# Performance work log

Measured on AMD Instinct MI355X. Metric: run time of the kernel, lower is better.

The kernel has to match this reference:

```python
import jax, jax.numpy as jnp
import numpy as np

B, S, D, H = 4, 2048, 512, 8
HD = D // H  # head dim = 64


def setup_inputs() -> dict:
    key = jax.random.key(0)
    ks = jax.random.split(key, 7)
    s = 0.02
    return {
        "X": jax.random.normal(ks[0], (B, S, D), dtype=jnp.float32),
        "Y": jax.random.normal(ks[1], (B, S, D), dtype=jnp.float32),
        "Z": jax.random.normal(ks[2], (B, S, D), dtype=jnp.float32),
        # weights stored as [in, out] (torch Linear weight transposed)
        "Wq": jax.random.normal(ks[3], (D, D), dtype=jnp.float32) * s,
        "Wk": jax.random.normal(ks[4], (D, D), dtype=jnp.float32) * s,
        "Wv": jax.random.normal(ks[5], (D, D), dtype=jnp.float32) * s,  # dead in original forward
        "Wo": jax.random.normal(ks[6], (D, D), dtype=jnp.float32) * s,
    }


def _split_heads(t):
    # [B, S, D] -> [B, H, S, HD]
    return t.reshape(B, S, H, HD).transpose(0, 2, 1, 3)


def reference(X, Y, Z, Wq, Wk, Wv, Wo):
    q = _split_heads(X @ Wq)
    k = _split_heads(Y @ Wk)
    # NOTE: original module (faithfully) uses W_o for the value projection; W_v is unused.
    v = _split_heads(Z @ Wo)
    scores = jnp.einsum("bhqd,bhkd->bhqk", q, k) / jnp.sqrt(jnp.float32(HD))
    # sigmoid(s) > 0.5  <=>  s > 0 (sigmoid strictly monotone); keep score else 0
    scores = jnp.where(scores > 0, scores, jnp.float32(0))
    attn = jax.nn.softmax(scores, axis=-1)
    out = jnp.einsum("bhqk,bhkd->bhqd", attn, v)  # dropout inactive at eval
    out = out.transpose(0, 2, 1, 3).reshape(B, S, D)  # merge heads
    return out @ Wo
```

## Files before the change

### kernel.cpp

```cpp
#include <hip/hip_runtime.h>
#include <math.h>

#define S_LEN 2048
#define DIM   512
#define M_TOT 8192
#define NCH   (S_LEN / 64)

typedef __attribute__((ext_vector_type(8))) short bf16x8;
typedef __attribute__((ext_vector_type(4))) short bf16x4;
typedef __attribute__((ext_vector_type(4))) float f32x4;

#define MFMA(a, b, c) __builtin_amdgcn_mfma_f32_16x16x32_bf16((a), (b), (c), 0, 0, 0)

#define QSCALE 0.18033688f

__device__ __forceinline__ short f2b(float x) {
    union { float f; unsigned u; } v; v.f = x;
    return (short)((v.u + 0x8000u) >> 16);
}
__device__ __forceinline__ int pack2(float x, float y) {
    union { float f; unsigned u; } a, b; a.f = x; b.f = y;
    return __builtin_amdgcn_perm(b.u + 0x8000u, a.u + 0x8000u, 0x07060302u);
}

__global__ __launch_bounds__(256) void cvt_bf16(const float* __restrict__ X,
                                                const float* __restrict__ Y,
                                                const float* __restrict__ Z,
                                                short* __restrict__ Xb,
                                                short* __restrict__ Yb,
                                                short* __restrict__ Zb) {
    const int zi = blockIdx.y;
    const float* A = zi == 0 ? X : zi == 1 ? Y : Z;
    short* O = zi == 0 ? Xb : zi == 1 ? Yb : Zb;
    const size_t i = (size_t)blockIdx.x * 256 + threadIdx.x;
    float4 a = ((const float4*)A)[2 * i];
    float4 b = ((const float4*)A)[2 * i + 1];
    int4 o = { pack2(a.x, a.y), pack2(a.z, a.w), pack2(b.x, b.y), pack2(b.z, b.w) };
    *(int4*)&O[i * 8] = o;
}

__global__ __launch_bounds__(256) void prep_wt(const float* Wq, const float* Wk, const float* Wo,
                                               short* Wtq, short* Wtk, short* Wto) {
    const int zi = blockIdx.z;
    const float* W = zi == 0 ? Wq : zi == 1 ? Wk : Wo;
    short*      Wt = zi == 0 ? Wtq : zi == 1 ? Wtk : Wto;
    __shared__ short Ts[64 * 72];
    const int t = threadIdx.x;
    const int k0 = blockIdx.x * 64, n0 = blockIdx.y * 64;
    #pragma unroll
    for (int it = 0; it < 4; ++it) {
        const int r = (t >> 4) + 16 * it;
        const int cq = t & 15;
        float4 v = *(const float4*)&W[(size_t)(k0 + r) * DIM + n0 + cq * 4];
        Ts[(4 * cq + 0) * 72 + r] = f2b(v.x);
        Ts[(4 * cq + 1) * 72 + r] = f2b(v.y);
        Ts[(4 * cq + 2) * 72 + r] = f2b(v.z);
        Ts[(4 * cq + 3) * 72 + r] = f2b(v.w);
    }
    __syncthreads();
    #pragma unroll
    for (int it = 0; it < 2; ++it) {
        const int n = (t >> 3) + 32 * it;
        const int sg = t & 7;
        *(bf16x8*)&Wt[(size_t)(n0 + n) * DIM + k0 + sg * 8] = *(const bf16x8*)&Ts[n * 72 + sg * 8];
    }
}

__global__ __launch_bounds__(256) void proj_gemm(const short* __restrict__ Xb,
                                                 const short* __restrict__ Yb,
                                                 const short* __restrict__ Zb,
                                                 const short* __restrict__ Wtq,
                                                 const short* __restrict__ Wtk,
                                                 const short* __restrict__ Wto,
                                                 short* __restrict__ Qb,
                                                 short* __restrict__ Kb,
                                                 short* __restrict__ Vt) {
    const int zi = blockIdx.z;
    const short* A  = zi == 0 ? Xb : zi == 1 ? Yb : Zb;
    const short* Bw = zi == 0 ? Wtq : zi == 1 ? Wtk : Wto;

    __shared__ short As[128 * 40];
    __shared__ short Bs[128 * 40];
    const int tid = threadIdx.x;
    const int w = tid >> 6, ln = tid & 63, l15 = ln & 15, quad = ln >> 4;
    const int m0 = blockIdx.x * 128, n0 = blockIdx.y * 128;
    const int wm = (w & 1) * 64, wn = (w >> 1) * 64;

    const int r0 = tid >> 2, r1 = r0 + 64;
    const int sg = tid & 3;
    const short* ap0 = A  + (size_t)(m0 + r0) * DIM + sg * 8;
    const short* ap1 = A  + (size_t)(m0 + r1) * DIM + sg * 8;
    const short* bp0 = Bw + (size_t)(n0 + r0) * DIM + sg * 8;
    const short* bp1 = Bw + (size_t)(n0 + r1) * DIM + sg * 8;

    bf16x8 a0 = *(const bf16x8*)ap0, a1 = *(const bf16x8*)ap1;
    bf16x8 b0 = *(const bf16x8*)bp0, b1 = *(const bf16x8*)bp1;

    f32x4 acc[4][4] = {};

    for (int k0 = 0; k0 < DIM; k0 += 32) {
        __syncthreads();
        *(bf16x8*)&As[r0 * 40 + sg * 8] = a0;
        *(bf16x8*)&As[r1 * 40 + sg * 8] = a1;
        *(bf16x8*)&Bs[r0 * 40 + sg * 8] = b0;
        *(bf16x8*)&Bs[r1 * 40 + sg * 8] = b1;
        __syncthreads();
        const int kn = (k0 + 32 < DIM) ? k0 + 32 : 0;
        a0 = *(const bf16x8*)(ap0 + kn); a1 = *(const bf16x8*)(ap1 + kn);
        b0 = *(const bf16x8*)(bp0 + kn); b1 = *(const bf16x8*)(bp1 + kn);

        bf16x8 af[4], bf[4];
        #pragma unroll
        for (int mf = 0; mf < 4; ++mf) af[mf] = *(const bf16x8*)&As[(wm + 16 * mf + l15) * 40 + quad * 8];
        #pragma unroll
        for (int nf = 0; nf < 4; ++nf) bf[nf] = *(const bf16x8*)&Bs[(wn + 16 * nf + l15) * 40 + quad * 8];
        #pragma unroll
        for (int mf = 0; mf < 4; ++mf)
            #pragma unroll
            for (int nf = 0; nf < 4; ++nf)
                acc[mf][nf] = MFMA(af[mf], bf[nf], acc[mf][nf]);
    }

    if (zi < 2) {
        short* C = zi == 0 ? Qb : Kb;
        const float scale = zi == 0 ? QSCALE : 1.0f;
        #pragma unroll
        for (int mf = 0; mf < 4; ++mf)
            #pragma unroll
            for (int nf = 0; nf < 4; ++nf) {
                int2 o = { pack2(acc[mf][nf][0] * scale, acc[mf][nf][1] * scale),
                           pack2(acc[mf][nf][2] * scale, acc[mf][nf][3] * scale) };
                C[(size_t)(m0 + wm + 16 * mf + 4 * quad + 0) * DIM + n0 + wn + 16 * nf + l15] = (short)(o.x & 0xFFFF);
                C[(size_t)(m0 + wm + 16 * mf + 4 * quad + 1) * DIM + n0 + wn + 16 * nf + l15] = (short)(o.x >> 16);
                C[(size_t)(m0 + wm + 16 * mf + 4 * quad + 2) * DIM + n0 + wn + 16 * nf + l15] = (short)(o.y & 0xFFFF);
                C[(size_t)(m0 + wm + 16 * mf + 4 * quad + 3) * DIM + n0 + wn + 16 * nf + l15] = (short)(o.y >> 16);
            }
    } else {
        #pragma unroll
        for (int mf = 0; mf < 4; ++mf)
            #pragma unroll
            for (int nf = 0; nf < 4; ++nf) {
                const int col = n0 + wn + 16 * nf + l15;
                const int h = col >> 6, hd = col & 63;
                const int row0_ = m0 + wm + 16 * mf + 4 * quad;
                const int bb = row0_ >> 11, s0 = row0_ & 2047;
                int2 o = { pack2(acc[mf][nf][0], acc[mf][nf][1]),
                           pack2(acc[mf][nf][2], acc[mf][nf][3]) };
                *(int2*)&Vt[((size_t)((bb * 8 + h) * 64 + hd)) * S_LEN + s0] = o;
            }
    }
}

__global__ __launch_bounds__(256) void out_gemm(const short* __restrict__ Ob,
                                                const short* __restrict__ Wto,
                                                float* __restrict__ Cout) {
    __shared__ short As[128 * 40];
    __shared__ short Bs[128 * 40];
    const int tid = threadIdx.x;
    const int w = tid >> 6, ln = tid & 63, l15 = ln & 15, quad = ln >> 4;
    const int m0 = blockIdx.x * 128, n0 = blockIdx.y * 128;
    const int wm = (w & 1) * 64, wn = (w >> 1) * 64;

    const int r0 = tid >> 2, r1 = r0 + 64;
    const int sg = tid & 3;
    const short* ap0 = Ob  + (size_t)(m0 + r0) * DIM + sg * 8;
    const short* ap1 = Ob  + (size_t)(m0 + r1) * DIM + sg * 8;
    const short* bp0 = Wto + (size_t)(n0 + r0) * DIM + sg * 8;
    const short* bp1 = Wto + (size_t)(n0 + r1) * DIM + sg * 8;

    bf16x8 a0 = *(const bf16x8*)ap0, a1 = *(const bf16x8*)ap1;
    bf16x8 b0 = *(const bf16x8*)bp0, b1 = *(const bf16x8*)bp1;

    f32x4 acc[4][4] = {};

    for (int k0 = 0; k0 < DIM; k0 += 32) {
        __syncthreads();
        *(bf16x8*)&As[r0 * 40 + sg * 8] = a0;
        *(bf16x8*)&As[r1 * 40 + sg * 8] = a1;
        *(bf16x8*)&Bs[r0 * 40 + sg * 8] = b0;
        *(bf16x8*)&Bs[r1 * 40 + sg * 8] = b1;
        __syncthreads();
        const int kn = (k0 + 32 < DIM) ? k0 + 32 : 0;
        a0 = *(const bf16x8*)(ap0 + kn); a1 = *(const bf16x8*)(ap1 + kn);
        b0 = *(const bf16x8*)(bp0 + kn); b1 = *(const bf16x8*)(bp1 + kn);

        bf16x8 af[4], bf[4];
        #pragma unroll
        for (int mf = 0; mf < 4; ++mf) af[mf] = *(const bf16x8*)&As[(wm + 16 * mf + l15) * 40 + quad * 8];
        #pragma unroll
        for (int nf = 0; nf < 4; ++nf) bf[nf] = *(const bf16x8*)&Bs[(wn + 16 * nf + l15) * 40 + quad * 8];
        #pragma unroll
        for (int mf = 0; mf < 4; ++mf)
            #pragma unroll
            for (int nf = 0; nf < 4; ++nf)
                acc[mf][nf] = MFMA(af[mf], bf[nf], acc[mf][nf]);
    }
    #pragma unroll
    for (int mf = 0; mf < 4; ++mf)
        #pragma unroll
        for (int nf = 0; nf < 4; ++nf)
            #pragma unroll
            for (int r = 0; r < 4; ++r)
                Cout[(size_t)(m0 + wm + 16 * mf + 4 * quad + r) * DIM + n0 + wn + 16 * nf + l15] =
                    acc[mf][nf][r];
}

__global__ __launch_bounds__(256) void attn_mfma(const short* __restrict__ Qb,
                                                 const short* __restrict__ Kb,
                                                 const short* __restrict__ Vtg,
                                                 short* __restrict__ Ob) {
    __shared__ short Ks[2][64 * 68];
    __shared__ short Vs[2][64 * 68];
    __shared__ short Es[4][32 * 68];

    const int tid = threadIdx.x;
    const int w = tid >> 6, ln = tid & 63, l15 = ln & 15, quad = ln >> 4;
    const int qt0 = blockIdx.x * 128;
    const int bh = blockIdx.y, b = bh >> 3, h = bh & 7;
    const size_t tokbase = (size_t)b * S_LEN;

    bf16x8 qf[2][2];
    #pragma unroll
    for (int nf = 0; nf < 2; ++nf)
        #pragma unroll
        for (int ks = 0; ks < 2; ++ks)
            qf[nf][ks] = *(const bf16x8*)&Qb[(tokbase + qt0 + 32 * w + 16 * nf + l15) * DIM +
                                             h * 64 + 32 * ks + 8 * quad];

    const int srow = tid >> 3, ssg = tid & 7;
    const short* kbase = Kb  + (tokbase + srow) * DIM + h * 64 + ssg * 8;
    const short* vbase = Vtg + ((size_t)bh * 64 + srow) * S_LEN + ssg * 8;

    const bf16x8 ones = { 0x3F80, 0x3F80, 0x3F80, 0x3F80, 0x3F80, 0x3F80, 0x3F80, 0x3F80 };

    f32x4 oacc[2][4] = {};
    f32x4 dacc[2] = {};

    bf16x8 kr0, kr1, vr0, vr1;
    kr0 = *(const bf16x8*)kbase;
    kr1 = *(const bf16x8*)(kbase + (size_t)32 * DIM);
    vr0 = *(const bf16x8*)vbase;
    vr1 = *(const bf16x8*)(vbase + (size_t)32 * S_LEN);
    *(bf16x8*)&Ks[0][srow * 68 + ssg * 8] = kr0;
    *(bf16x8*)&Ks[0][(srow + 32) * 68 + ssg * 8] = kr1;
    *(bf16x8*)&Vs[0][srow * 68 + ssg * 8] = vr0;
    *(bf16x8*)&Vs[0][(srow + 32) * 68 + ssg * 8] = vr1;
    kr0 = *(const bf16x8*)(kbase + (size_t)64 * DIM);
    kr1 = *(const bf16x8*)(kbase + (size_t)96 * DIM);
    vr0 = *(const bf16x8*)(vbase + 64);
    vr1 = *(const bf16x8*)(vbase + (size_t)32 * S_LEN + 64);
    __syncthreads();

    for (int kc = 0; kc < NCH; ++kc) {
        const int cur = kc & 1;
        if (kc + 1 < NCH) {
            *(bf16x8*)&Ks[cur ^ 1][srow * 68 + ssg * 8] = kr0;
            *(bf16x8*)&Ks[cur ^ 1][(srow + 32) * 68 + ssg * 8] = kr1;
            *(bf16x8*)&Vs[cur ^ 1][srow * 68 + ssg * 8] = vr0;
            *(bf16x8*)&Vs[cur ^ 1][(srow + 32) * 68 + ssg * 8] = vr1;
        }
        if (kc + 2 < NCH) {
            const size_t ko = (size_t)(kc + 2) * 64 * DIM;
            const size_t vo = (size_t)(kc + 2) * 64;
            kr0 = *(const bf16x8*)(kbase + ko);
            kr1 = *(const bf16x8*)(kbase + ko + (size_t)32 * DIM);
            vr0 = *(const bf16x8*)(vbase + vo);
            vr1 = *(const bf16x8*)(vbase + vo + (size_t)32 * S_LEN);
        }

        f32x4 sacc[4][2];
        #pragma unroll
        for (int mf = 0; mf < 4; ++mf) {
            bf16x8 ka  = *(const bf16x8*)&Ks[cur][(16 * mf + l15) * 68 + 8 * quad];
            bf16x8 kb2 = *(const bf16x8*)&Ks[cur][(16 * mf + l15) * 68 + 32 + 8 * quad];
            #pragma unroll
            for (int nf = 0; nf < 2; ++nf) {
                f32x4 s = {0.f, 0.f, 0.f, 0.f};
                s = MFMA(ka, qf[nf][0], s);
                s = MFMA(kb2, qf[nf][1], s);
                sacc[mf][nf] = s;
            }
        }

        short* Esw = &Es[w][0];
        #pragma unroll
        for (int mf = 0; mf < 4; ++mf)
            #pragma unroll
            for (int nf = 0; nf < 2; ++nf) {
                float e0 = __builtin_amdgcn_exp2f(fmaxf(sacc[mf][nf][0], 0.f));
                float e1 = __builtin_amdgcn_exp2f(fmaxf(sacc[mf][nf][1], 0.f));
                float e2 = __builtin_amdgcn_exp2f(fmaxf(sacc[mf][nf][2], 0.f));
                float e3 = __builtin_amdgcn_exp2f(fmaxf(sacc[mf][nf][3], 0.f));
                int2 p = { pack2(e0, e1), pack2(e2, e3) };
                *(int2*)&Esw[(16 * nf + l15) * 68 + 16 * mf + 4 * quad] = p;
            }

        bf16x8 e[2][2];
        #pragma unroll
        for (int nf = 0; nf < 2; ++nf) {
            e[nf][0] = *(const bf16x8*)&Esw[(16 * nf + l15) * 68 + 8 * quad];
            e[nf][1] = *(const bf16x8*)&Esw[(16 * nf + l15) * 68 + 32 + 8 * quad];
            dacc[nf] = MFMA(e[nf][0], ones, dacc[nf]);
            dacc[nf] = MFMA(e[nf][1], ones, dacc[nf]);
        }
        #pragma unroll
        for (int nf2 = 0; nf2 < 4; ++nf2) {
            bf16x8 vf0 = *(const bf16x8*)&Vs[cur][(16 * nf2 + l15) * 68 + 8 * quad];
            bf16x8 vf1 = *(const bf16x8*)&Vs[cur][(16 * nf2 + l15) * 68 + 32 + 8 * quad];
            #pragma unroll
            for (int nf = 0; nf < 2; ++nf) {
                oacc[nf][nf2] = MFMA(e[nf][0], vf0, oacc[nf][nf2]);
                oacc[nf][nf2] = MFMA(e[nf][1], vf1, oacc[nf][nf2]);
            }
        }
        __syncthreads();
    }

    #pragma unroll
    for (int nf = 0; nf < 2; ++nf)
        #pragma unroll
        for (int r = 0; r < 4; ++r) {
            const float di = __builtin_amdgcn_rcpf(dacc[nf][r]);
            const size_t rowaddr = (tokbase + qt0 + 32 * w + 16 * nf + 4 * quad + r) * DIM + h * 64;
            #pragma unroll
            for (int nf2 = 0; nf2 < 4; ++nf2)
                Ob[rowaddr + 16 * nf2 + l15] = f2b(oacc[nf][nf2][r] * di);
        }
}

extern "C" void kernel_launch(void* const* d_in, const int* in_sizes, int n_in,
                              void* d_out, int out_size, void* d_ws, size_t ws_size,
                              hipStream_t stream) {
    const float* X  = (const float*)d_in[0];
    const float* Y  = (const float*)d_in[1];
    const float* Z  = (const float*)d_in[2];
    const float* Wq = (const float*)d_in[3];
    const float* Wk = (const float*)d_in[4];
    const float* Wo = (const float*)d_in[6];

    char* p = (char*)d_ws;
    const size_t MD = (size_t)M_TOT * DIM;
    short* Qb  = (short*)p; p += MD * 2;
    short* Kb  = (short*)p; p += MD * 2;
    short* Vt  = (short*)p; p += MD * 2;
    short* Ob  = (short*)p; p += MD * 2;
    short* Xb  = (short*)p; p += MD * 2;
    short* Yb  = (short*)p; p += MD * 2;
    short* Zb  = (short*)p; p += MD * 2;
    short* Wtq = (short*)p; p += (size_t)DIM * DIM * 2;
    short* Wtk = (short*)p; p += (size_t)DIM * DIM * 2;
    short* Wto = (short*)p; p += (size_t)DIM * DIM * 2;

    cvt_bf16<<<dim3(M_TOT * DIM / 8 / 256, 3), 256, 0, stream>>>(X, Y, Z, Xb, Yb, Zb);
    prep_wt<<<dim3(8, 8, 3), 256, 0, stream>>>(Wq, Wk, Wo, Wtq, Wtk, Wto);
    proj_gemm<<<dim3(64, 4, 3), 256, 0, stream>>>(Xb, Yb, Zb, Wtq, Wtk, Wto, Qb, Kb, Vt);
    attn_mfma<<<dim3(16, 32), 256, 0, stream>>>(Qb, Kb, Vt, Ob);
    out_gemm<<<dim3(64, 4), 256, 0, stream>>>(Ob, Wto, (float*)d_out);
}
```

Baseline: 221.5 us.

## Split attention over key halves with combine pass; fuse fp32-to-bf16 into projection

The attention kernel now splits the key range into two halves across a third grid dimension. Each half writes unnormalized fp32 partial outputs and denominators, and a new combine kernel sums them, normalizes, and writes bf16 output. This doubles the block count (512 to 1024) to fill more CUs, at the cost of extra fp32 traffic and one more launch. The separate input conversion kernel is removed: proj_gemm reads fp32 inputs directly and packs them to bf16 while staging into shared memory. The K/V double buffering in attention is replaced by single-buffered LDS staging, and the combine output reuses the Q buffer.

```diff
diff --git a/kernel.cpp b/kernel.cpp
--- a/kernel.cpp
+++ b/kernel.cpp
@@ -4,7 +4,8 @@
 #define S_LEN 2048
 #define DIM   512
 #define M_TOT 8192
-#define NCH   (S_LEN / 64)
+#define KSPLIT 2
+#define NCH2  (S_LEN / 64 / KSPLIT)
 
 typedef __attribute__((ext_vector_type(8))) short bf16x8;
 typedef __attribute__((ext_vector_type(4))) short bf16x4;
@@ -21,22 +22,6 @@
 __device__ __forceinline__ int pack2(float x, float y) {
     union { float f; unsigned u; } a, b; a.f = x; b.f = y;
     return __builtin_amdgcn_perm(b.u + 0x8000u, a.u + 0x8000u, 0x07060302u);
-}
-
-__global__ __launch_bounds__(256) void cvt_bf16(const float* __restrict__ X,
-                                                const float* __restrict__ Y,
-                                                const float* __restrict__ Z,
-                                                short* __restrict__ Xb,
-                                                short* __restrict__ Yb,
-                                                short* __restrict__ Zb) {
-    const int zi = blockIdx.y;
-    const float* A = zi == 0 ? X : zi == 1 ? Y : Z;
-    short* O = zi == 0 ? Xb : zi == 1 ? Yb : Zb;
-    const size_t i = (size_t)blockIdx.x * 256 + threadIdx.x;
-    float4 a = ((const float4*)A)[2 * i];
-    float4 b = ((const float4*)A)[2 * i + 1];
-    int4 o = { pack2(a.x, a.y), pack2(a.z, a.w), pack2(b.x, b.y), pack2(b.z, b.w) };
-    *(int4*)&O[i * 8] = o;
 }
 
 __global__ __launch_bounds__(256) void prep_wt(const float* Wq, const float* Wk, const float* Wo,
@@ -66,9 +51,9 @@
     }
 }
 
-__global__ __launch_bounds__(256) void proj_gemm(const short* __restrict__ Xb,
-                                                 const short* __restrict__ Yb,
-                                                 const short* __restrict__ Zb,
+__global__ __launch_bounds__(256) void proj_gemm(const float* __restrict__ X,
+                                                 const float* __restrict__ Y,
+                                                 const float* __restrict__ Z,
                                                  const short* __restrict__ Wtq,
                                                  const short* __restrict__ Wtk,
                                                  const short* __restrict__ Wto,
@@ -76,7 +61,7 @@
                                                  short* __restrict__ Kb,
                                                  short* __restrict__ Vt) {
     const int zi = blockIdx.z;
-    const short* A  = zi == 0 ? Xb : zi == 1 ? Yb : Zb;
+    const float* A  = zi == 0 ? X : zi == 1 ? Y : Z;
     const short* Bw = zi == 0 ? Wtq : zi == 1 ? Wtk : Wto;
 
     __shared__ short As[128 * 40];
@@ -88,25 +73,33 @@
 
     const int r0 = tid >> 2, r1 = r0 + 64;
     const int sg = tid & 3;
-    const short* ap0 = A  + (size_t)(m0 + r0) * DIM + sg * 8;
-    const short* ap1 = A  + (size_t)(m0 + r1) * DIM + sg * 8;
+    const float* ap0 = A  + (size_t)(m0 + r0) * DIM + sg * 8;
+    const float* ap1 = A  + (size_t)(m0 + r1) * DIM + sg * 8;
     const short* bp0 = Bw + (size_t)(n0 + r0) * DIM + sg * 8;
     const short* bp1 = Bw + (size_t)(n0 + r1) * DIM + sg * 8;
 
-    bf16x8 a0 = *(const bf16x8*)ap0, a1 = *(const bf16x8*)ap1;
+    float4 a0a = *(const float4*)ap0, a0b = *(const float4*)(ap0 + 4);
+    float4 a1a = *(const float4*)ap1, a1b = *(const float4*)(ap1 + 4);
     bf16x8 b0 = *(const bf16x8*)bp0, b1 = *(const bf16x8*)bp1;
 
     f32x4 acc[4][4] = {};
 
     for (int k0 = 0; k0 < DIM; k0 += 32) {
         __syncthreads();
-        *(bf16x8*)&As[r0 * 40 + sg * 8] = a0;
-        *(bf16x8*)&As[r1 * 40 + sg * 8] = a1;
-        *(bf16x8*)&Bs[r0 * 40 + sg * 8] = b0;
-        *(bf16x8*)&Bs[r1 * 40 + sg * 8] = b1;
+        {
+            int4 p0 = { pack2(a0a.x, a0a.y), pack2(a0a.z, a0a.w),
+                        pack2(a0b.x, a0b.y), pack2(a0b.z, a0b.w) };
+            int4 p1 = { pack2(a1a.x, a1a.y), pack2(a1a.z, a1a.w),
+                        pack2(a1b.x, a1b.y), pack2(a1b.z, a1b.w) };
+            *(int4*)&As[r0 * 40 + sg * 8] = p0;
+            *(int4*)&As[r1 * 40 + sg * 8] = p1;
+            *(bf16x8*)&Bs[r0 * 40 + sg * 8] = b0;
+            *(bf16x8*)&Bs[r1 * 40 + sg * 8] = b1;
+        }
         __syncthreads();
         const int kn = (k0 + 32 < DIM) ? k0 + 32 : 0;
-        a0 = *(const bf16x8*)(ap0 + kn); a1 = *(const bf16x8*)(ap1 + kn);
+        a0a = *(const float4*)(ap0 + kn); a0b = *(const float4*)(ap0 + kn + 4);
+        a1a = *(const float4*)(ap1 + kn); a1b = *(const float4*)(ap1 + kn + 4);
         b0 = *(const bf16x8*)(bp0 + kn); b1 = *(const bf16x8*)(bp1 + kn);
 
         bf16x8 af[4], bf[4];
@@ -127,14 +120,11 @@
         #pragma unroll
         for (int mf = 0; mf < 4; ++mf)
             #pragma unroll
-            for (int nf = 0; nf < 4; ++nf) {
-                int2 o = { pack2(acc[mf][nf][0] * scale, acc[mf][nf][1] * scale),
-                           pack2(acc[mf][nf][2] * scale, acc[mf][nf][3] * scale) };
-                C[(size_t)(m0 + wm + 16 * mf + 4 * quad + 0) * DIM + n0 + wn + 16 * nf + l15] = (short)(o.x & 0xFFFF);
-                C[(size_t)(m0 + wm + 16 * mf + 4 * quad + 1) * DIM + n0 + wn + 16 * nf + l15] = (short)(o.x >> 16);
-                C[(size_t)(m0 + wm + 16 * mf + 4 * quad + 2) * DIM + n0 + wn + 16 * nf + l15] = (short)(o.y & 0xFFFF);
-                C[(size_t)(m0 + wm + 16 * mf + 4 * quad + 3) * DIM + n0 + wn + 16 * nf + l15] = (short)(o.y >> 16);
-            }
+            for (int nf = 0; nf < 4; ++nf)
+                #pragma unroll
+                for (int r = 0; r < 4; ++r)
+                    C[(size_t)(m0 + wm + 16 * mf + 4 * quad + r) * DIM + n0 + wn + 16 * nf + l15] =
+                        f2b(acc[mf][nf][r] * scale);
     } else {
         #pragma unroll
         for (int mf = 0; mf < 4; ++mf)
@@ -208,16 +198,19 @@
 __global__ __launch_bounds__(256) void attn_mfma(const short* __restrict__ Qb,
                                                  const short* __restrict__ Kb,
                                                  const short* __restrict__ Vtg,
-                                                 short* __restrict__ Ob) {
-    __shared__ short Ks[2][64 * 68];
-    __shared__ short Vs[2][64 * 68];
+                                                 float* __restrict__ Opart,
+                                                 float* __restrict__ Dpart) {
+    __shared__ short Ks[64 * 68];
+    __shared__ short Vs[64 * 68];
     __shared__ short Es[4][32 * 68];
 
     const int tid = threadIdx.x;
     const int w = tid >> 6, ln = tid & 63, l15 = ln & 15, quad = ln >> 4;
     const int qt0 = blockIdx.x * 128;
     const int bh = blockIdx.y, b = bh >> 3, h = bh & 7;
+    const int kp = blockIdx.z;
     const size_t tokbase = (size_t)b * S_LEN;
+    const int key0 = kp * (S_LEN / KSPLIT);
 
     bf16x8 qf[2][2];
     #pragma unroll
@@ -228,40 +221,29 @@
                                              h * 64 + 32 * ks + 8 * quad];
 
     const int srow = tid >> 3, ssg = tid & 7;
-    const short* kbase = Kb  + (tokbase + srow) * DIM + h * 64 + ssg * 8;
-    const short* vbase = Vtg + ((size_t)bh * 64 + srow) * S_LEN + ssg * 8;
+    const short* kbase = Kb  + (tokbase + key0 + srow) * DIM + h * 64 + ssg * 8;
+    const short* vbase = Vtg + ((size_t)bh * 64 + srow) * S_LEN + key0 + ssg * 8;
 
     const bf16x8 ones = { 0x3F80, 0x3F80, 0x3F80, 0x3F80, 0x3F80, 0x3F80, 0x3F80, 0x3F80 };
 
     f32x4 oacc[2][4] = {};
     f32x4 dacc[2] = {};
 
-    bf16x8 kr0, kr1, vr0, vr1;
-    kr0 = *(const bf16x8*)kbase;
-    kr1 = *(const bf16x8*)(kbase + (size_t)32 * DIM);
-    vr0 = *(const bf16x8*)vbase;
-    vr1 = *(const bf16x8*)(vbase + (size_t)32 * S_LEN);
-    *(bf16x8*)&Ks[0][srow * 68 + ssg * 8] = kr0;
-    *(bf16x8*)&Ks[0][(srow + 32) * 68 + ssg * 8] = kr1;
-    *(bf16x8*)&Vs[0][srow * 68 + ssg * 8] = vr0;
-    *(bf16x8*)&Vs[0][(srow + 32) * 68 + ssg * 8] = vr1;
-    kr0 = *(const bf16x8*)(kbase + (size_t)64 * DIM);
-    kr1 = *(const bf16x8*)(kbase + (size_t)96 * DIM);
-    vr0 = *(const bf16x8*)(vbase + 64);
-    vr1 = *(const bf16x8*)(vbase + (size_t)32 * S_LEN + 64);
-    __syncthreads();
-
-    for (int kc = 0; kc < NCH; ++kc) {
-        const int cur = kc & 1;
-        if (kc + 1 < NCH) {
-            *(bf16x8*)&Ks[cur ^ 1][srow * 68 + ssg * 8] = kr0;
-            *(bf16x8*)&Ks[cur ^ 1][(srow + 32) * 68 + ssg * 8] = kr1;
-            *(bf16x8*)&Vs[cur ^ 1][srow * 68 + ssg * 8] = vr0;
-            *(bf16x8*)&Vs[cur ^ 1][(srow + 32) * 68 + ssg * 8] = vr1;
-        }
-        if (kc + 2 < NCH) {
-            const size_t ko = (size_t)(kc + 2) * 64 * DIM;
-            const size_t vo = (size_t)(kc + 2) * 64;
+    bf16x8 kr0 = *(const bf16x8*)kbase;
+    bf16x8 kr1 = *(const bf16x8*)(kbase + (size_t)32 * DIM);
+    bf16x8 vr0 = *(const bf16x8*)vbase;
+    bf16x8 vr1 = *(const bf16x8*)(vbase + (size_t)32 * S_LEN);
+
+    for (int kc = 0; kc < NCH2; ++kc) {
+        __syncthreads();
+        *(bf16x8*)&Ks[srow * 68 + ssg * 8] = kr0;
+        *(bf16x8*)&Ks[(srow + 32) * 68 + ssg * 8] = kr1;
+        *(bf16x8*)&Vs[srow * 68 + ssg * 8] = vr0;
+        *(bf16x8*)&Vs[(srow + 32) * 68 + ssg * 8] = vr1;
+        __syncthreads();
+        if (kc + 1 < NCH2) {
+            const size_t ko = (size_t)(kc + 1) * 64 * DIM;
+            const size_t vo = (size_t)(kc + 1) * 64;
             kr0 = *(const bf16x8*)(kbase + ko);
             kr1 = *(const bf16x8*)(kbase + ko + (size_t)32 * DIM);
             vr0 = *(const bf16x8*)(vbase + vo);
@@ -271,8 +253,8 @@
         f32x4 sacc[4][2];
         #pragma unroll
         for (int mf = 0; mf < 4; ++mf) {
-            bf16x8 ka  = *(const bf16x8*)&Ks[cur][(16 * mf + l15) * 68 + 8 * quad];
-            bf16x8 kb2 = *(const bf16x8*)&Ks[cur][(16 * mf + l15) * 68 + 32 + 8 * quad];
+            bf16x8 ka  = *(const bf16x8*)&Ks[(16 * mf + l15) * 68 + 8 * quad];
+            bf16x8 kb2 = *(const bf16x8*)&Ks[(16 * mf + l15) * 68 + 32 + 8 * quad];
             #pragma unroll
             for (int nf = 0; nf < 2; ++nf) {
                 f32x4 s = {0.f, 0.f, 0.f, 0.f};
@@ -305,27 +287,46 @@
         }
         #pragma unroll
         for (int nf2 = 0; nf2 < 4; ++nf2) {
-            bf16x8 vf0 = *(const bf16x8*)&Vs[cur][(16 * nf2 + l15) * 68 + 8 * quad];
-            bf16x8 vf1 = *(const bf16x8*)&Vs[cur][(16 * nf2 + l15) * 68 + 32 + 8 * quad];
+            bf16x8 vf0 = *(const bf16x8*)&Vs[(16 * nf2 + l15) * 68 + 8 * quad];
+            bf16x8 vf1 = *(const bf16x8*)&Vs[(16 * nf2 + l15) * 68 + 32 + 8 * quad];
             #pragma unroll
             for (int nf = 0; nf < 2; ++nf) {
                 oacc[nf][nf2] = MFMA(e[nf][0], vf0, oacc[nf][nf2]);
                 oacc[nf][nf2] = MFMA(e[nf][1], vf1, oacc[nf][nf2]);
             }
         }
-        __syncthreads();
-    }
-
+    }
+
+    float* obase = Opart + ((size_t)kp * 32 + bh) * ((size_t)S_LEN * 64);
+    float* dbase = Dpart + ((size_t)kp * 32 + bh) * S_LEN;
     #pragma unroll
     for (int nf = 0; nf < 2; ++nf)
         #pragma unroll
         for (int r = 0; r < 4; ++r) {
-            const float di = __builtin_amdgcn_rcpf(dacc[nf][r]);
-            const size_t rowaddr = (tokbase + qt0 + 32 * w + 16 * nf + 4 * quad + r) * DIM + h * 64;
+            const int qg = qt0 + 32 * w + 16 * nf + 4 * quad + r;
             #pragma unroll
             for (int nf2 = 0; nf2 < 4; ++nf2)
-                Ob[rowaddr + 16 * nf2 + l15] = f2b(oacc[nf][nf2][r] * di);
-        }
+                obase[(size_t)qg * 64 + 16 * nf2 + l15] = oacc[nf][nf2][r];
+            if (l15 == 0) dbase[qg] = dacc[nf][r];
+        }
+}
+
+__global__ __launch_bounds__(256) void combine(const float* __restrict__ Opart,
+                                               const float* __restrict__ Dpart,
+                                               short* __restrict__ Ob) {
+    const int g = blockIdx.x * 256 + threadIdx.x;
+    const int row = g >> 4;
+    const int hq = (g & 15) << 2;
+    const size_t PLANE = (size_t)32 * S_LEN * 64;
+    float4 n0 = *(const float4*)&Opart[(size_t)row * 64 + hq];
+    float4 n1 = *(const float4*)&Opart[PLANE + (size_t)row * 64 + hq];
+    const float den = Dpart[row] + Dpart[32 * S_LEN + row];
+    const float rv = __builtin_amdgcn_rcpf(den);
+    const int bh = row >> 11, q = row & 2047;
+    const int b = bh >> 3, h = bh & 7;
+    int2 o = { pack2((n0.x + n1.x) * rv, (n0.y + n1.y) * rv),
+               pack2((n0.z + n1.z) * rv, (n0.w + n1.w) * rv) };
+    *(int2*)&Ob[((size_t)(b * S_LEN + q)) * DIM + h * 64 + hq] = o;
 }
 
 extern "C" void kernel_launch(void* const* d_in, const int* in_sizes, int n_in,
@@ -343,17 +344,16 @@
     short* Qb  = (short*)p; p += MD * 2;
     short* Kb  = (short*)p; p += MD * 2;
     short* Vt  = (short*)p; p += MD * 2;
-    short* Ob  = (short*)p; p += MD * 2;
-    short* Xb  = (short*)p; p += MD * 2;
-    short* Yb  = (short*)p; p += MD * 2;
-    short* Zb  = (short*)p; p += MD * 2;
     short* Wtq = (short*)p; p += (size_t)DIM * DIM * 2;
     short* Wtk = (short*)p; p += (size_t)DIM * DIM * 2;
     short* Wto = (short*)p; p += (size_t)DIM * DIM * 2;
-
-    cvt_bf16<<<dim3(M_TOT * DIM / 8 / 256, 3), 256, 0, stream>>>(X, Y, Z, Xb, Yb, Zb);
+    float* Opart = (float*)p; p += (size_t)KSPLIT * 32 * S_LEN * 64 * 4;
+    float* Dpart = (float*)p; p += (size_t)KSPLIT * 32 * S_LEN * 4;
+    short* Ob = Qb;
+
     prep_wt<<<dim3(8, 8, 3), 256, 0, stream>>>(Wq, Wk, Wo, Wtq, Wtk, Wto);
-    proj_gemm<<<dim3(64, 4, 3), 256, 0, stream>>>(Xb, Yb, Zb, Wtq, Wtk, Wto, Qb, Kb, Vt);
-    attn_mfma<<<dim3(16, 32), 256, 0, stream>>>(Qb, Kb, Vt, Ob);
+    proj_gemm<<<dim3(64, 4, 3), 256, 0, stream>>>(X, Y, Z, Wtq, Wtk, Wto, Qb, Kb, Vt);
+    attn_mfma<<<dim3(16, 32, KSPLIT), 256, 0, stream>>>(Qb, Kb, Vt, Opart, Dpart);
+    combine<<<dim3(M_TOT * DIM / 4 / 256), 256, 0, stream>>>(Opart, Dpart, Ob);
     out_gemm<<<dim3(64, 4), 256, 0, stream>>>(Ob, Wto, (float*)d_out);
 }
```

New measurement: 242.4 us. 9.4% more time.
